# Kernel optimization log

Measured on AMD Instinct MI355X. Metric: run time of the kernel, lower is better.

Reference implementation:

```python
import jax, jax.numpy as jnp
import numpy as np

NUM_HEADS = 16
HEAD_DIM = 64  # embedding_dim 1024 / 16


def setup_inputs() -> dict:
    key = jax.random.key(0)
    k1, k2, k3, k4 = jax.random.split(key, 4)
    B, S, D = 2, 2048, 1024
    return {
        "query": jax.random.normal(k1, (B, S, D), dtype=jnp.float32),
        "key": jax.random.normal(k2, (B, S, D), dtype=jnp.float32),
        "value": jax.random.normal(k3, (B, S, D), dtype=jnp.float32),
        "W_out": jax.random.normal(k4, (D, D), dtype=jnp.float32) * (1.0 / np.sqrt(D)),
        "b_out": jnp.zeros((D,), dtype=jnp.float32),
    }


def reference(query, key, value, W_out, b_out):
    B, S, D = query.shape
    H, hd = NUM_HEADS, HEAD_DIM
    # NOTE: original forward never applies q_fc/k_fc/v_fc (transform ignores fc)
    q = query.reshape(B, S, H, hd).transpose(0, 2, 1, 3)  # [B,H,S,hd]
    k = key.reshape(B, S, H, hd).transpose(0, 2, 1, 3)
    v = value.reshape(B, S, H, hd).transpose(0, 2, 1, 3)
    scores = jnp.einsum("bhqd,bhkd->bhqk", q, k) / jnp.sqrt(jnp.float32(hd))
    probs = jax.nn.softmax(scores, axis=-1)  # mask=None, dropout=None
    ctx = jnp.einsum("bhqk,bhkd->bhqd", probs, v)
    ctx = ctx.transpose(0, 2, 1, 3).reshape(B, S, D)
    return ctx @ W_out.T + b_out
```

## Files before the change

### kernel.cpp

```cpp
#include <hip/hip_runtime.h>
#include <hip/hip_bf16.h>
#include <stdint.h>

#define NB 2
#define SEQ 2048
#define DIM 1024
#define NH 16
#define HD 64

typedef __attribute__((ext_vector_type(4))) float f32x4;
typedef __attribute__((ext_vector_type(16))) float f32x16;
typedef __attribute__((ext_vector_type(8))) short s16x8;
typedef __attribute__((ext_vector_type(4))) short s16x4;
typedef __attribute__((ext_vector_type(8))) __bf16 bf16x8;

static __device__ __forceinline__ short f2bf_rne(float x) {
  uint32_t u = __float_as_uint(x);
  u += 0x7fffu + ((u >> 16) & 1u);
  return (short)(u >> 16);
}
static __device__ __forceinline__ uint32_t pk_bf16(float a, float b) {
  __hip_bfloat162 h = __float22bfloat162_rn(float2{a, b});
  uint32_t u;
  __builtin_memcpy(&u, &h, 4);
  return u;
}
static __device__ __forceinline__ bf16x8 ldfrag(const short* p) {
  bf16x8 r;
  __builtin_memcpy(&r, p, 16);
  return r;
}
static __device__ __forceinline__ void glds16(const short* g, short* l) {
  __builtin_amdgcn_global_load_lds(
      (const __attribute__((address_space(1))) uint32_t*)g,
      (__attribute__((address_space(3))) uint32_t*)l, 16, 0, 0);
}

__global__ __launch_bounds__(256) void prep_all(const float* __restrict__ K,
                                                const float* __restrict__ V,
                                                const float* __restrict__ W,
                                                short* __restrict__ Kh,
                                                short* __restrict__ Vt,
                                                short* __restrict__ Wh) {
  __shared__ float vtile[64][65];
  const int tid = threadIdx.x;
  const int id = blockIdx.x;

  if (id >= 1024) {
    size_t idx = ((size_t)(id - 1024) * 256 + tid) * 8;
    f32x4 a = *(const f32x4*)(W + idx);
    f32x4 b = *(const f32x4*)(W + idx + 4);
    s16x8 o;
#pragma unroll
    for (int j = 0; j < 4; ++j) {
      o[j] = f2bf_rne(a[j]);
      o[4 + j] = f2bf_rne(b[j]);
    }
    *(s16x8*)(Wh + idx) = o;
    return;
  }

  const int t0 = (id & 31) * 64;
  const int bh = id >> 5;
  const int b = bh >> 4, h = bh & 15;

#pragma unroll
  for (int i = 0; i < 4; ++i) {
    int f = tid + 256 * i;
    int row = f >> 4;
    int col = (f & 15) * 4;
    const float* src = K + ((size_t)(b * SEQ + t0 + row)) * DIM + h * HD + col;
    f32x4 v = *(const f32x4*)src;
    s16x4 hi;
#pragma unroll
    for (int j = 0; j < 4; ++j) hi[j] = f2bf_rne(v[j]);
    *(s16x4*)(Kh + ((size_t)bh * SEQ + t0 + row) * HD + col) = hi;
  }
#pragma unroll
  for (int i = 0; i < 4; ++i) {
    int f = tid + 256 * i;
    int row = f >> 4;
    int col = (f & 15) * 4;
    const float* src = V + ((size_t)(b * SEQ + t0 + row)) * DIM + h * HD + col;
    f32x4 v = *(const f32x4*)src;
#pragma unroll
    for (int j = 0; j < 4; ++j) vtile[row][col + j] = v[j];
  }
  __syncthreads();
#pragma unroll
  for (int i = 0; i < 4; ++i) {
    int idx = tid + 256 * i;
    int d = idx >> 4;
    int kb = (idx & 15) * 4;
    int kp = (kb & ~12) | ((kb & 4) << 1) | ((kb & 8) >> 1);
    s16x4 o4;
#pragma unroll
    for (int j = 0; j < 4; ++j) o4[j] = f2bf_rne(vtile[kb + j][d]);
    *(s16x4*)(Vt + ((size_t)bh * HD + d) * SEQ + t0 + kp) = o4;
  }
}

#define QSCALE (0.125f * 1.44269504088896340736f)
#define NT_KV 32

__global__ __launch_bounds__(256, 2) void attn(const float* __restrict__ Q,
                                               const short* __restrict__ Kh,
                                               const short* __restrict__ Vt,
                                               short* __restrict__ Ch) {
  __shared__ __align__(16) short kbuf[2][4096];
  __shared__ __align__(16) short vbuf[2][4096];

  const int tid = threadIdx.x;
  const int wv = tid >> 6, ln = tid & 63;
  const int l32 = ln & 31, hl = ln >> 5;
  const int bh = blockIdx.y, b = bh >> 4, hh = bh & 15;
  const int q0 = blockIdx.x * 128 + wv * 32;

  bf16x8 qh[4];
  {
    const float* qp = Q + ((size_t)(b * SEQ + q0 + l32)) * DIM + hh * HD + hl * 8;
#pragma unroll
    for (int ks = 0; ks < 4; ++ks) {
      short th[8];
#pragma unroll
      for (int j = 0; j < 8; ++j) th[j] = f2bf_rne(qp[ks * 16 + j] * QSCALE);
      __builtin_memcpy(&qh[ks], th, 16);
    }
  }

  f32x16 acc[2];
#pragma unroll
  for (int r = 0; r < 16; ++r) {
    acc[0][r] = 0.f;
    acc[1][r] = 0.f;
  }
  float den0 = 0.f, den1 = 0.f;

  const short* khg = Kh + (size_t)bh * SEQ * HD;
  const short* vtg = Vt + (size_t)bh * HD * SEQ;

  const int srow8 = ln >> 3;
  const int sg = ln & 7;
  const int sw = (sg ^ srow8) * 8;

#pragma unroll
  for (int i = 0; i < 6; ++i) {
    int c = wv * 6 + i;
    int lc = c & 7;
    int row = lc * 8 + srow8;
    if (c < 8)
      glds16(khg + (size_t)row * HD + sw, &kbuf[0][lc * 512]);
    else if (c < 16)
      glds16(vtg + (size_t)row * SEQ + sw, &vbuf[0][lc * 512]);
    else
      glds16(khg + (size_t)(64 + row) * HD + sw, &kbuf[1][lc * 512]);
  }
  __syncthreads();

  f32x16 sf[2];
#pragma unroll
  for (int nt = 0; nt < 2; ++nt) {
#pragma unroll
    for (int r = 0; r < 16; ++r) sf[nt][r] = 0.f;
#pragma unroll
    for (int ks = 0; ks < 4; ++ks) {
      bf16x8 kf = ldfrag(&kbuf[0][0] + (nt * 32 + l32) * 64 +
                         (((ks * 2 + hl) ^ (l32 & 7)) * 8));
      sf[nt] = __builtin_amdgcn_mfma_f32_32x32x16_bf16(kf, qh[ks], sf[nt], 0, 0, 0);
    }
  }

  for (int t = 0; t < NT_KV; ++t) {
    __syncthreads();
    if (t + 2 < NT_KV) {
      const int kvn = (t + 2) * 64;
#pragma unroll
      for (int i = 0; i < 2; ++i) {
        int lc = wv * 2 + i;
        int row = lc * 8 + srow8;
        glds16(khg + (size_t)(kvn + row) * HD + sw, &kbuf[t & 1][lc * 512]);
      }
    }
    if (t + 1 < NT_KV) {
      const int kvn = (t + 1) * 64;
#pragma unroll
      for (int i = 0; i < 2; ++i) {
        int lc = wv * 2 + i;
        int row = lc * 8 + srow8;
        glds16(vtg + (size_t)row * SEQ + kvn + sw, &vbuf[(t + 1) & 1][lc * 512]);
      }
    }
    const short* kbn = &kbuf[(t + 1) & 1][0];
    const short* vbc = &vbuf[t & 1][0];

#pragma unroll
    for (int nt = 0; nt < 2; ++nt) {
      f32x16 sfn;
      if (t + 1 < NT_KV) {
#pragma unroll
        for (int r = 0; r < 16; ++r) sfn[r] = 0.f;
#pragma unroll
        for (int ks = 0; ks < 4; ++ks) {
          bf16x8 kf = ldfrag(kbn + (nt * 32 + l32) * 64 +
                             (((ks * 2 + hl) ^ (l32 & 7)) * 8));
          sfn = __builtin_amdgcn_mfma_f32_32x32x16_bf16(kf, qh[ks], sfn, 0, 0, 0);
        }
      }
#pragma unroll
      for (int tp = 0; tp < 2; ++tp) {
        uint32_t w[4];
#pragma unroll
        for (int j2 = 0; j2 < 4; ++j2) {
          float p0 = __builtin_amdgcn_exp2f(sf[nt][tp * 8 + j2 * 2]);
          float p1 = __builtin_amdgcn_exp2f(sf[nt][tp * 8 + j2 * 2 + 1]);
          den0 += p0;
          den1 += p1;
          w[j2] = pk_bf16(p0, p1);
        }
        bf16x8 pa;
        __builtin_memcpy(&pa, w, 16);
        const int ksg = nt * 2 + tp;
#pragma unroll
        for (int dt = 0; dt < 2; ++dt) {
          bf16x8 vf = ldfrag(vbc + (dt * 32 + l32) * 64 +
                             (((ksg * 2 + hl) ^ (l32 & 7)) * 8));
          acc[dt] =
              __builtin_amdgcn_mfma_f32_32x32x16_bf16(pa, vf, acc[dt], 0, 0, 0);
        }
      }
      if (t + 1 < NT_KV) sf[nt] = sfn;
    }
  }

  float den = den0 + den1;
  den += __shfl_xor(den, 32);
  float invd = 1.0f / den;
  float inv_r[16];
#pragma unroll
  for (int r = 0; r < 16; ++r)
    inv_r[r] = __shfl(invd, (r & 3) + 8 * (r >> 2) + 4 * hl, 64);
#pragma unroll
  for (int dt = 0; dt < 2; ++dt)
#pragma unroll
    for (int r = 0; r < 16; ++r) {
      int row = (r & 3) + 8 * (r >> 2) + 4 * hl;
      size_t off = ((size_t)(b * SEQ + q0 + row)) * DIM + hh * HD + dt * 32 + l32;
      Ch[off] = f2bf_rne(acc[dt][r] * inv_r[r]);
    }
}

__global__ __launch_bounds__(256, 4) void proj(const short* __restrict__ Ah,
                                               const short* __restrict__ Wh,
                                               const float* __restrict__ bias,
                                               float* __restrict__ OUT) {
  __shared__ __align__(16) short ash[2][4096];
  __shared__ __align__(16) short wsh[2][4096];
  const int tid = threadIdx.x;
  const int wv = tid >> 6, ln = tid & 63;
  const int l32 = ln & 31, hl = ln >> 5;
  const int wm = wv & 1, wn = wv >> 1;
  const int m0 = blockIdx.x * 64, n0 = blockIdx.y * 64;

  f32x16 acc;
#pragma unroll
  for (int r = 0; r < 16; ++r) acc[r] = 0.f;

  const int srow8 = ln >> 3, sg = ln & 7;
  const int sw = (sg ^ srow8) * 8;

#pragma unroll
  for (int i = 0; i < 4; ++i) {
    int c = wv * 4 + i;
    int row = (c & 7) * 8 + srow8;
    if (c < 8)
      glds16(Ah + (size_t)(m0 + row) * DIM + sw, ash[0] + (c & 7) * 512);
    else
      glds16(Wh + (size_t)(n0 + row) * DIM + sw, wsh[0] + (c & 7) * 512);
  }

  for (int kt = 0; kt < DIM / 64; ++kt) {
    __syncthreads();
    if (kt + 1 < DIM / 64) {
      const int kk = (kt + 1) * 64;
      const int bn = (kt + 1) & 1;
#pragma unroll
      for (int i = 0; i < 4; ++i) {
        int c = wv * 4 + i;
        int row = (c & 7) * 8 + srow8;
        if (c < 8)
          glds16(Ah + (size_t)(m0 + row) * DIM + kk + sw, ash[bn] + (c & 7) * 512);
        else
          glds16(Wh + (size_t)(n0 + row) * DIM + kk + sw, wsh[bn] + (c & 7) * 512);
      }
    }
    const short* ab = ash[kt & 1];
    const short* wb = wsh[kt & 1];
#pragma unroll
    for (int ks = 0; ks < 4; ++ks) {
      bf16x8 af = ldfrag(ab + (wm * 32 + l32) * 64 + (((ks * 2 + hl) ^ (l32 & 7)) * 8));
      bf16x8 wf = ldfrag(wb + (wn * 32 + l32) * 64 + (((ks * 2 + hl) ^ (l32 & 7)) * 8));
      acc = __builtin_amdgcn_mfma_f32_32x32x16_bf16(af, wf, acc, 0, 0, 0);
    }
  }

  float bs = bias[n0 + wn * 32 + l32];
#pragma unroll
  for (int r = 0; r < 16; ++r) {
    int row = m0 + wm * 32 + (r & 3) + 8 * (r >> 2) + 4 * hl;
    int col = n0 + wn * 32 + l32;
    OUT[(size_t)row * DIM + col] = acc[r] + bs;
  }
}

extern "C" void kernel_launch(void* const* d_in, const int* in_sizes, int n_in,
                              void* d_out, int out_size, void* d_ws, size_t ws_size,
                              hipStream_t stream) {
  const float* Q = (const float*)d_in[0];
  const float* K = (const float*)d_in[1];
  const float* V = (const float*)d_in[2];
  const float* W = (const float*)d_in[3];
  const float* bias = (const float*)d_in[4];
  float* OUT = (float*)d_out;

  char* ws = (char*)d_ws;
  short* Kh = (short*)(ws + ((size_t)0 << 20));
  short* Vt = (short*)(ws + ((size_t)8 << 20));
  short* Ch = (short*)(ws + ((size_t)16 << 20));
  short* Wh = (short*)(ws + ((size_t)24 << 20));

  prep_all<<<dim3(1536), 256, 0, stream>>>(K, V, W, Kh, Vt, Wh);
  attn<<<dim3(SEQ / 128, NB * NH), 256, 0, stream>>>(Q, Kh, Vt, Ch);
  proj<<<dim3((NB * SEQ) / 64, DIM / 64), 256, 0, stream>>>(Ch, Wh, bias, OUT);
}
```

Baseline: 159.0 us.

## Split attention KV tiles across wave pairs with 512-thread blocks and LDS reduction

The attention kernel doubles its block to 8 waves. Each pair of waves shares 32 query rows, and within a pair each wave handles one 32-key half of every 64-key KV tile. The partial PV accumulators and softmax denominators are exchanged through LDS at the end and summed, with each wave writing one 32-column half of the output. The KV loop is also manually unrolled by two with ping-pong buffers and less loading work per wave. The aim is more waves in flight and fewer serial MFMA chains per wave to hide latency, at the cost of an extra LDS reduction, more barriers and higher register pressure from the 512-thread launch bounds.

New measurement: 369.8 us. 2.33x slower.

```diff
diff --git a/kernel.cpp b/kernel.cpp
--- a/kernel.cpp
+++ b/kernel.cpp
@@ -103,18 +103,62 @@
 #define QSCALE (0.125f * 1.44269504088896340736f)
 #define NT_KV 32
 
-__global__ __launch_bounds__(256, 2) void attn(const float* __restrict__ Q,
+static __device__ __forceinline__ f32x16 qk32(const short* kb, int kvh, int l32,
+                                              int hl, const bf16x8* qh) {
+  f32x16 s;
+#pragma unroll
+  for (int r = 0; r < 16; ++r) s[r] = 0.f;
+#pragma unroll
+  for (int ks = 0; ks < 4; ++ks) {
+    bf16x8 kf =
+        ldfrag(kb + (kvh * 32 + l32) * 64 + (((ks * 2 + hl) ^ (l32 & 7)) * 8));
+    s = __builtin_amdgcn_mfma_f32_32x32x16_bf16(kf, qh[ks], s, 0, 0, 0);
+  }
+  return s;
+}
+
+static __device__ __forceinline__ void exppv32(const f32x16& sf, const short* vb,
+                                               int kvh, int l32, int hl,
+                                               f32x16* acc, float& den0,
+                                               float& den1) {
+#pragma unroll
+  for (int tp = 0; tp < 2; ++tp) {
+    uint32_t w[4];
+#pragma unroll
+    for (int j2 = 0; j2 < 4; ++j2) {
+      float p0 = __builtin_amdgcn_exp2f(sf[tp * 8 + j2 * 2]);
+      float p1 = __builtin_amdgcn_exp2f(sf[tp * 8 + j2 * 2 + 1]);
+      den0 += p0;
+      den1 += p1;
+      w[j2] = pk_bf16(p0, p1);
+    }
+    bf16x8 pa;
+    __builtin_memcpy(&pa, w, 16);
+    const int ksg = kvh * 2 + tp;
+#pragma unroll
+    for (int dt = 0; dt < 2; ++dt) {
+      bf16x8 vf = ldfrag(vb + (dt * 32 + l32) * 64 +
+                         (((ksg * 2 + hl) ^ (l32 & 7)) * 8));
+      acc[dt] =
+          __builtin_amdgcn_mfma_f32_32x32x16_bf16(pa, vf, acc[dt], 0, 0, 0);
+    }
+  }
+}
+
+__global__ __launch_bounds__(512, 4) void attn(const float* __restrict__ Q,
                                                const short* __restrict__ Kh,
                                                const short* __restrict__ Vt,
                                                short* __restrict__ Ch) {
   __shared__ __align__(16) short kbuf[2][4096];
   __shared__ __align__(16) short vbuf[2][4096];
+  __shared__ float dsh[8][64];
 
   const int tid = threadIdx.x;
   const int wv = tid >> 6, ln = tid & 63;
   const int l32 = ln & 31, hl = ln >> 5;
+  const int qsub = wv >> 1, kvh = wv & 1;
   const int bh = blockIdx.y, b = bh >> 4, hh = bh & 15;
-  const int q0 = blockIdx.x * 128 + wv * 32;
+  const int q0 = blockIdx.x * 128 + qsub * 32;
 
   bf16x8 qh[4];
   {
@@ -144,8 +188,8 @@
   const int sw = (sg ^ srow8) * 8;
 
 #pragma unroll
-  for (int i = 0; i < 6; ++i) {
-    int c = wv * 6 + i;
+  for (int i = 0; i < 3; ++i) {
+    int c = wv * 3 + i;
     int lc = c & 7;
     int row = lc * 8 + srow8;
     if (c < 8)
@@ -157,96 +201,57 @@
   }
   __syncthreads();
 
-  f32x16 sf[2];
-#pragma unroll
-  for (int nt = 0; nt < 2; ++nt) {
-#pragma unroll
-    for (int r = 0; r < 16; ++r) sf[nt][r] = 0.f;
-#pragma unroll
-    for (int ks = 0; ks < 4; ++ks) {
-      bf16x8 kf = ldfrag(&kbuf[0][0] + (nt * 32 + l32) * 64 +
-                         (((ks * 2 + hl) ^ (l32 & 7)) * 8));
-      sf[nt] = __builtin_amdgcn_mfma_f32_32x32x16_bf16(kf, qh[ks], sf[nt], 0, 0, 0);
-    }
-  }
-
-  for (int t = 0; t < NT_KV; ++t) {
+  f32x16 sfA = qk32(&kbuf[0][0], kvh, l32, hl, qh);
+
+  const int srow = wv * 8 + srow8;
+
+  for (int t = 0; t < 30; t += 2) {
     __syncthreads();
-    if (t + 2 < NT_KV) {
-      const int kvn = (t + 2) * 64;
-#pragma unroll
-      for (int i = 0; i < 2; ++i) {
-        int lc = wv * 2 + i;
-        int row = lc * 8 + srow8;
-        glds16(khg + (size_t)(kvn + row) * HD + sw, &kbuf[t & 1][lc * 512]);
-      }
-    }
-    if (t + 1 < NT_KV) {
-      const int kvn = (t + 1) * 64;
-#pragma unroll
-      for (int i = 0; i < 2; ++i) {
-        int lc = wv * 2 + i;
-        int row = lc * 8 + srow8;
-        glds16(vtg + (size_t)row * SEQ + kvn + sw, &vbuf[(t + 1) & 1][lc * 512]);
-      }
-    }
-    const short* kbn = &kbuf[(t + 1) & 1][0];
-    const short* vbc = &vbuf[t & 1][0];
-
-#pragma unroll
-    for (int nt = 0; nt < 2; ++nt) {
-      f32x16 sfn;
-      if (t + 1 < NT_KV) {
-#pragma unroll
-        for (int r = 0; r < 16; ++r) sfn[r] = 0.f;
-#pragma unroll
-        for (int ks = 0; ks < 4; ++ks) {
-          bf16x8 kf = ldfrag(kbn + (nt * 32 + l32) * 64 +
-                             (((ks * 2 + hl) ^ (l32 & 7)) * 8));
-          sfn = __builtin_amdgcn_mfma_f32_32x32x16_bf16(kf, qh[ks], sfn, 0, 0, 0);
-        }
-      }
-#pragma unroll
-      for (int tp = 0; tp < 2; ++tp) {
-        uint32_t w[4];
-#pragma unroll
-        for (int j2 = 0; j2 < 4; ++j2) {
-          float p0 = __builtin_amdgcn_exp2f(sf[nt][tp * 8 + j2 * 2]);
-          float p1 = __builtin_amdgcn_exp2f(sf[nt][tp * 8 + j2 * 2 + 1]);
-          den0 += p0;
-          den1 += p1;
-          w[j2] = pk_bf16(p0, p1);
-        }
-        bf16x8 pa;
-        __builtin_memcpy(&pa, w, 16);
-        const int ksg = nt * 2 + tp;
-#pragma unroll
-        for (int dt = 0; dt < 2; ++dt) {
-          bf16x8 vf = ldfrag(vbc + (dt * 32 + l32) * 64 +
-                             (((ksg * 2 + hl) ^ (l32 & 7)) * 8));
-          acc[dt] =
-              __builtin_amdgcn_mfma_f32_32x32x16_bf16(pa, vf, acc[dt], 0, 0, 0);
-        }
-      }
-      if (t + 1 < NT_KV) sf[nt] = sfn;
-    }
-  }
+    glds16(khg + (size_t)((t + 2) * 64 + srow) * HD + sw, &kbuf[0][wv * 512]);
+    glds16(vtg + (size_t)srow * SEQ + (t + 1) * 64 + sw, &vbuf[1][wv * 512]);
+    f32x16 sfB = qk32(&kbuf[1][0], kvh, l32, hl, qh);
+    exppv32(sfA, &vbuf[0][0], kvh, l32, hl, acc, den0, den1);
+    __syncthreads();
+    glds16(khg + (size_t)((t + 3) * 64 + srow) * HD + sw, &kbuf[1][wv * 512]);
+    glds16(vtg + (size_t)srow * SEQ + (t + 2) * 64 + sw, &vbuf[0][wv * 512]);
+    sfA = qk32(&kbuf[0][0], kvh, l32, hl, qh);
+    exppv32(sfB, &vbuf[1][0], kvh, l32, hl, acc, den0, den1);
+  }
+  __syncthreads();
+  glds16(vtg + (size_t)srow * SEQ + 31 * 64 + sw, &vbuf[1][wv * 512]);
+  f32x16 sfT = qk32(&kbuf[1][0], kvh, l32, hl, qh);
+  exppv32(sfA, &vbuf[0][0], kvh, l32, hl, acc, den0, den1);
+  __syncthreads();
+  exppv32(sfT, &vbuf[1][0], kvh, l32, hl, acc, den0, den1);
 
   float den = den0 + den1;
   den += __shfl_xor(den, 32);
-  float invd = 1.0f / den;
+
+  __syncthreads();
+  float* xr = (wv < 4) ? (float*)&kbuf[0][0] : (float*)&vbuf[0][0];
+  float* xs = xr + (wv & 3) * 1024 + ln * 16;
+  __builtin_memcpy(xs, &acc[kvh ^ 1], 64);
+  dsh[wv][ln] = den;
+  __syncthreads();
+
+  float dtot = den + dsh[wv ^ 1][ln];
+  float invd = 1.0f / dtot;
   float inv_r[16];
 #pragma unroll
   for (int r = 0; r < 16; ++r)
     inv_r[r] = __shfl(invd, (r & 3) + 8 * (r >> 2) + 4 * hl, 64);
-#pragma unroll
-  for (int dt = 0; dt < 2; ++dt)
-#pragma unroll
-    for (int r = 0; r < 16; ++r) {
-      int row = (r & 3) + 8 * (r >> 2) + 4 * hl;
-      size_t off = ((size_t)(b * SEQ + q0 + row)) * DIM + hh * HD + dt * 32 + l32;
-      Ch[off] = f2bf_rne(acc[dt][r] * inv_r[r]);
-    }
+
+  f32x16 oth;
+  const float* xo = xr + ((wv ^ 1) & 3) * 1024 + ln * 16;
+  __builtin_memcpy(&oth, xo, 64);
+#pragma unroll
+  for (int r = 0; r < 16; ++r) {
+    float cs = acc[kvh][r] + oth[r];
+    int row = (r & 3) + 8 * (r >> 2) + 4 * hl;
+    size_t off =
+        ((size_t)(b * SEQ + q0 + row)) * DIM + hh * HD + kvh * 32 + l32;
+    Ch[off] = f2bf_rne(cs * inv_r[r]);
+  }
 }
 
 __global__ __launch_bounds__(256, 4) void proj(const short* __restrict__ Ah,
@@ -329,6 +334,6 @@
   short* Wh = (short*)(ws + ((size_t)24 << 20));
 
   prep_all<<<dim3(1536), 256, 0, stream>>>(K, V, W, Kh, Vt, Wh);
-  attn<<<dim3(SEQ / 128, NB * NH), 256, 0, stream>>>(Q, Kh, Vt, Ch);
+  attn<<<dim3(SEQ / 128, NB * NH), 512, 0, stream>>>(Q, Kh, Vt, Ch);
   proj<<<dim3((NB * SEQ) / 64, DIM / 64), 256, 0, stream>>>(Ch, Wh, bias, OUT);
 }
```
